# Performance work log

Measured on AMD Instinct MI355X. Metric: run time of the kernel, lower is better.

Reference implementation:

```python
import jax, jax.numpy as jnp
import numpy as np

NEG_INF = -9e15
ALPHA = 0.2  # attention leaky_relu slope


def _gat_layer(h, adj_mask, W, a1, a2):
    # h: [N, Fin], W: [Fin, D], a1/a2: [D]
    Wh = h @ W                                   # [N, D]
    f1 = Wh @ a1                                 # [N]
    f2 = Wh @ a2                                 # [N]
    e = jax.nn.leaky_relu(f1[:, None] + f2[None, :], ALPHA)  # [N, N]
    scores = jnp.where(adj_mask, e, NEG_INF)
    att = jax.nn.softmax(scores, axis=-1)        # row-normalized over neighbors
    return att @ Wh                              # [N, D]


def setup_inputs() -> dict:
    key = jax.random.key(0)
    ks = jax.random.split(key, 12)
    N, Fin, H, D, C = 4096, 512, 8, 64, 64
    s = 0.1
    x = jax.random.normal(ks[0], (N, Fin), jnp.float32)
    adj = jax.random.randint(ks[1], (N, N), 0, 2, jnp.int32)
    W = jax.random.normal(ks[2], (H, Fin, D), jnp.float32) * s
    a1 = jax.random.normal(ks[3], (H, D), jnp.float32) * s
    a2 = jax.random.normal(ks[4], (H, D), jnp.float32) * s
    Wo = jax.random.normal(ks[5], (H * D, C), jnp.float32) * s
    ao1 = jax.random.normal(ks[6], (C,), jnp.float32) * s
    ao2 = jax.random.normal(ks[7], (C,), jnp.float32) * s
    W1 = jax.random.normal(ks[8], (512, N), jnp.float32) * 0.01  # nn.Linear(N, 512)
    b1 = jnp.zeros((512,), jnp.float32)
    W2 = jax.random.normal(ks[9], (256, 512), jnp.float32) * 0.04  # nn.Linear(512, 256)
    b2 = jnp.zeros((256,), jnp.float32)
    return {"x": x, "adj": adj, "W": W, "a1": a1, "a2": a2,
            "Wo": Wo, "ao1": ao1, "ao2": ao2,
            "W1": W1, "b1": b1, "W2": W2, "b2": b2}


def reference(x, adj, W, a1, a2, Wo, ao1, ao2, W1, b1, W2, b2):
    mask = adj > 0                                    # [N, N]
    # multi-head dense attention, concat=True -> ELU per head
    heads = jax.vmap(lambda Wk, a1k, a2k: _gat_layer(x, mask, Wk, a1k, a2k))(W, a1, a2)  # [H, N, D]
    h = jax.nn.elu(heads).transpose(1, 0, 2).reshape(x.shape[0], -1)  # [N, H*D]
    # output attention layer, concat=False (no inner ELU), then outer ELU
    out = jax.nn.elu(_gat_layer(h, mask, Wo, ao1, ao2))  # [N, C]
    out = jax.nn.log_softmax(out, axis=0)                # over nodes (dim=0)
    # MLP head on transposed features: [C, N] -> [C, 512] -> [C, 256]
    y = jax.nn.leaky_relu(out.T @ W1.T + b1, 0.1)
    y = y @ W2.T + b2
    return y
```

## Files before the change

kernel.cpp:

```cpp
#include <hip/hip_runtime.h>
#include <hip/hip_bf16.h>
#include <math.h>


#define N_NODES 4096
#define FIN 512
#define NHEAD 8
#define DHEAD 64
#define NCLS 64
#define NW 64

typedef unsigned short u16;
typedef unsigned long long u64;
typedef __attribute__((ext_vector_type(8))) short bf16x8;
typedef __attribute__((ext_vector_type(4))) float f32x4;

__device__ __forceinline__ float lrelu02(float x) { return x > 0.f ? x : 0.2f * x; }
__device__ __forceinline__ u16 bf16u(float x) {
    __hip_bfloat16 h = __float2bfloat16(x);
    return __builtin_bit_cast(unsigned short, h);
}
__device__ __forceinline__ f32x4 mfma16(bf16x8 a, bf16x8 b, f32x4 c) {
    return __builtin_amdgcn_mfma_f32_16x16x32_bf16(a, b, c, 0, 0, 0);
}
__device__ __forceinline__ unsigned fkey(float f) {
    unsigned u = __builtin_bit_cast(unsigned, f);
    return (u & 0x80000000u) ? ~u : (u | 0x80000000u);
}
__device__ __forceinline__ float funkey(unsigned k) {
    unsigned u = (k & 0x80000000u) ? (k ^ 0x80000000u) : ~k;
    return __builtin_bit_cast(float, u);
}

__global__ void pack_mask(const int* __restrict__ adj, u64* __restrict__ mb,
                          unsigned* __restrict__ gmk) {
    if (blockIdx.x == 0 && threadIdx.x < 16) gmk[threadIdx.x] = 0u;
    int nwaves = (gridDim.x * blockDim.x) >> 6;
    int wid = (blockIdx.x * blockDim.x + threadIdx.x) >> 6;
    int lane = threadIdx.x & 63;
    for (int w = wid; w < N_NODES * NW; w += nwaves) {
        int i = w >> 6, wc = w & 63;
        int j = (wc << 6) | lane;
        u64 m = __ballot(adj[(size_t)i * N_NODES + j] > 0);
        if (lane == 0) mb[w] = m;
    }
}

__global__ void cvt4(const float* __restrict__ s, u16* __restrict__ d, int n4) {
    int i = blockIdx.x * blockDim.x + threadIdx.x;
    if (i < n4) {
        float4 v = ((const float4*)s)[i];
        ushort4 o = {bf16u(v.x), bf16u(v.y), bf16u(v.z), bf16u(v.w)};
        ((ushort4*)d)[i] = o;
    }
}

__global__ __launch_bounds__(256) void to_bf16_T(
    const float* __restrict__ src, int ldsrc, size_t cstep,
    u16* __restrict__ dst, size_t dstep, int ldd) {
    __shared__ alignas(16) u16 T[64][72];
    const int j0 = blockIdx.x * 64;
    const size_t c0 = (size_t)blockIdx.y * cstep;
    u16* d = dst + (size_t)blockIdx.y * dstep;
    const int t = threadIdx.x;
    const int row = t & 63, g = t >> 6;
    #pragma unroll
    for (int k = 0; k < 16; k += 4) {
        float4 v = *(const float4*)(src + (size_t)(j0 + row) * ldsrc + c0 + g * 16 + k);
        T[g * 16 + k + 0][row] = bf16u(v.x);
        T[g * 16 + k + 1][row] = bf16u(v.y);
        T[g * 16 + k + 2][row] = bf16u(v.z);
        T[g * 16 + k + 3][row] = bf16u(v.w);
    }
    __syncthreads();
    const int dd = t >> 2, jc = (t & 3) * 16;
    *(uint4*)(d + (size_t)dd * ldd + j0 + jc) = *(const uint4*)&T[dd][jc];
    *(uint4*)(d + (size_t)dd * ldd + j0 + jc + 8) = *(const uint4*)&T[dd][jc + 8];
}

__global__ __launch_bounds__(256) void gemm_fused(
    const u16* __restrict__ A, int lda, const u16* __restrict__ Bt, int ldb,
    const float* __restrict__ a1a, const float* __restrict__ a2a,
    u16* __restrict__ WhBT, float* __restrict__ f1o, float* __restrict__ f2o,
    unsigned* __restrict__ gmk, int K) {
    __shared__ alignas(16) u16 T[64][72];
    const int t = threadIdx.x, lane = t & 63, wv = t >> 6;
    const int c16 = lane & 15, kg = lane >> 4;
    const int h = blockIdx.x;
    const int bm = blockIdx.y * 64;
    const u16* Ap = A + (size_t)(bm + wv * 16 + c16) * lda + kg * 8;
    const u16* Bp = Bt + (size_t)(h * 64 + c16) * ldb + kg * 8;
    f32x4 acc[4] = {};
    #pragma unroll 4
    for (int k0 = 0; k0 < K; k0 += 32) {
        bf16x8 a = *(const bf16x8*)(Ap + k0);
        #pragma unroll
        for (int ct = 0; ct < 4; ++ct) {
            bf16x8 b = *(const bf16x8*)(Bp + (size_t)ct * 16 * ldb + k0);
            acc[ct] = mfma16(a, b, acc[ct]);
        }
    }
    float a1v[4], a2v[4];
    #pragma unroll
    for (int ct = 0; ct < 4; ++ct) {
        a1v[ct] = a1a[h * 64 + ct * 16 + c16];
        a2v[ct] = a2a[h * 64 + ct * 16 + c16];
    }
    float mx = -1e30f;
    #pragma unroll
    for (int r = 0; r < 4; ++r) {
        float s1 = 0.f, s2 = 0.f;
        int rl = wv * 16 + kg * 4 + r;
        #pragma unroll
        for (int ct = 0; ct < 4; ++ct) {
            float v = acc[ct][r];
            s1 = fmaf(v, a1v[ct], s1);
            s2 = fmaf(v, a2v[ct], s2);
            T[ct * 16 + c16][rl] = bf16u(v);
        }
        #pragma unroll
        for (int off = 1; off < 16; off <<= 1) {
            s1 += __shfl_xor(s1, off, 64);
            s2 += __shfl_xor(s2, off, 64);
        }
        if (c16 == 0) {
            f1o[(size_t)h * N_NODES + bm + rl] = s1;
            f2o[(size_t)h * N_NODES + bm + rl] = s2;
        }
        mx = fmaxf(mx, s2);
    }
    mx = fmaxf(mx, __shfl_xor(mx, 16, 64));
    mx = fmaxf(mx, __shfl_xor(mx, 32, 64));
    if (lane == 0) atomicMax(&gmk[h], fkey(mx));
    __syncthreads();
    const int dd = t >> 2, jc = (t & 3) * 16;
    u16* dst = WhBT + (size_t)(h * 64 + dd) * N_NODES + bm;
    *(uint4*)(dst + jc) = *(const uint4*)&T[dd][jc];
    *(uint4*)(dst + jc + 8) = *(const uint4*)&T[dd][jc + 8];
}

__global__ void coefk(const float* __restrict__ f1, const float* __restrict__ f2,
                      const unsigned* __restrict__ gmk, float4* __restrict__ rowc,
                      float2* __restrict__ uv) {
    int h = blockIdx.y;
    int i = blockIdx.x * 256 + threadIdx.x;
    float g = funkey(gmk[h]);
    float a = f1[(size_t)h * N_NODES + i];
    float s = a + g;
    float M = lrelu02(s);
    rowc[(size_t)h * N_NODES + i] = make_float4(__expf(s - M), __expf(0.2f * s - M), 0.f, 0.f);
    float b = f2[(size_t)h * N_NODES + i] - g;
    uv[(size_t)h * N_NODES + i] = make_float2(__expf(b), __expf(0.2f * b));
}

template <int NH, int ROWS, int JSPLIT, int OUTF>
__global__ __launch_bounds__(256) void attn_v3(
    const u16* __restrict__ WhB, const float2* __restrict__ uv,
    const float4* __restrict__ rowc, const u64* __restrict__ mb,
    float* __restrict__ outp, float* __restrict__ denP) {
    constexpr int NQ = ROWS / 4;
    constexpr int NMT = ROWS / 16;
    constexpr int NJT = (N_NODES / 64) / JSPLIT;
    __shared__ alignas(16) u16 pS[2][ROWS][64];
    __shared__ float Tof[(OUTF == 3) ? 64 * 33 : 1];
    const int b = blockIdx.x;
    int h, ib, js;
    if (NH == 8) { h = b & 7; int r = b >> 3; js = r % JSPLIT; ib = r / JSPLIT; }
    else { h = 0; js = b % JSPLIT; ib = b / JSPLIT; }
    const int i0 = ib * ROWS;
    const int jt0 = js * NJT;
    const int t = threadIdx.x, lane = t & 63, wv = t >> 6;
    const int wv_u = __builtin_amdgcn_readfirstlane(wv);

    const float2* __restrict__ uvp = uv + (size_t)h * N_NODES;
    const float4* __restrict__ rcp = rowc + (size_t)h * N_NODES;
    const u64* __restrict__ mbp = mb + (size_t)(i0 + wv_u) * NW + jt0;

    float Aq[NQ], Bq[NQ], den[NQ];
    #pragma unroll
    for (int q = 0; q < NQ; ++q) {
        float4 rc = rcp[i0 + q * 4 + wv];
        Aq[q] = rc.x; Bq[q] = rc.y; den[q] = 0.f;
    }
    const int wcE = lane ^ (wv << 3);
    const int wcO = lane ^ ((wv + 4) << 3);
    const int kg = lane >> 4, c16 = lane & 15;
    const int ocol = wv * 16 + c16;
    const u16* bptr = WhB + ((size_t)h * 64 + ocol) * N_NODES + jt0 * 64 + kg * 8;
    const int sw8 = (c16 & 7) << 3;
    f32x4 acc[NMT] = {};

    bf16x8 b0 = *(const bf16x8*)(bptr);
    bf16x8 b1 = *(const bf16x8*)(bptr + 32);
    float2 uvv = uvp[jt0 * 64 + lane];
    u64 m[NQ];
    #pragma unroll
    for (int q = 0; q < NQ; ++q) m[q] = mbp[q * 4 * NW];

    for (int it = 0; it < NJT; ++it) {
        const int buf = it & 1;
        const int nit = (it + 1 < NJT) ? it + 1 : it;
        bf16x8 nb0 = *(const bf16x8*)(bptr + (size_t)nit * 64);
        bf16x8 nb1 = *(const bf16x8*)(bptr + (size_t)nit * 64 + 32);
        float2 nuv = uvp[(jt0 + nit) * 64 + lane];
        u64 nm[NQ];
        #pragma unroll
        for (int q = 0; q < NQ; ++q) nm[q] = mbp[q * 4 * NW + nit];
        #pragma unroll
        for (int q = 0; q < NQ; ++q) {
            unsigned wlo = __builtin_amdgcn_readfirstlane((unsigned)m[q]);
            unsigned whi = __builtin_amdgcn_readfirstlane((unsigned)(m[q] >> 32));
            u64 ws = ((u64)whi << 32) | wlo;
            float tv = fmaxf(Aq[q] * uvv.x, Bq[q] * uvv.y);
            float p;
            asm("v_cndmask_b32 %0, 0, %1, %2" : "=v"(p) : "v"(tv), "s"(ws));
            den[q] += p;
            pS[buf][q * 4 + wv][(q & 1) ? wcO : wcE] = bf16u(p);
        }
        __syncthreads();
        __builtin_amdgcn_s_setprio(1);
        #pragma unroll
        for (int mt = 0; mt < NMT; ++mt) {
            const u16* ap = &pS[buf][mt * 16 + c16][0];
            bf16x8 a0 = *(const bf16x8*)&ap[(kg * 8) ^ sw8];
            bf16x8 a1 = *(const bf16x8*)&ap[(32 + kg * 8) ^ sw8];
            acc[mt] = mfma16(a0, b0, acc[mt]);
            acc[mt] = mfma16(a1, b1, acc[mt]);
        }
        __builtin_amdgcn_s_setprio(0);
        b0 = nb0; b1 = nb1; uvv = nuv;
        #pragma unroll
        for (int q = 0; q < NQ; ++q) m[q] = nm[q];
    }

    #pragma unroll
    for (int q = 0; q < NQ; ++q) {
        float s = den[q];
        #pragma unroll
        for (int off = 32; off; off >>= 1) s += __shfl_xor(s, off, 64);
        den[q] = s;
    }

    if constexpr (OUTF == 1) {
        if (lane == 0) {
            #pragma unroll
            for (int q = 0; q < NQ; ++q)
                denP[(size_t)js * (8 * N_NODES) + (size_t)h * N_NODES + i0 + q * 4 + wv] = den[q];
        }
        float* dst = outp + (size_t)js * N_NODES * 512;
        #pragma unroll
        for (int mt = 0; mt < NMT; ++mt)
            #pragma unroll
            for (int r = 0; r < 4; ++r)
                dst[(size_t)(i0 + mt * 16 + kg * 4 + r) * 512 + h * 64 + ocol] = acc[mt][r];
    } else {
        if (lane == 0) {
            #pragma unroll
            for (int q = 0; q < NQ; ++q)
                denP[(size_t)js * N_NODES + i0 + q * 4 + wv] = den[q];
        }
        #pragma unroll
        for (int mt = 0; mt < NMT; ++mt)
            #pragma unroll
            for (int r = 0; r < 4; ++r)
                Tof[ocol * 33 + mt * 16 + kg * 4 + r] = acc[mt][r];
        __syncthreads();
        const int c = t >> 2, r0 = (t & 3) * 8;
        float* dst = outp + (size_t)js * 64 * N_NODES + (size_t)c * N_NODES + i0 + r0;
        float4 v0 = {Tof[c * 33 + r0 + 0], Tof[c * 33 + r0 + 1],
                     Tof[c * 33 + r0 + 2], Tof[c * 33 + r0 + 3]};
        float4 v1 = {Tof[c * 33 + r0 + 4], Tof[c * 33 + r0 + 5],
                     Tof[c * 33 + r0 + 6], Tof[c * 33 + r0 + 7]};
        *(float4*)(dst) = v0;
        *(float4*)(dst + 4) = v1;
    }
}

__global__ __launch_bounds__(256) void combine8(
    const float* __restrict__ part, const float* __restrict__ denp,
    u16* __restrict__ hB) {
    const int t4 = (blockIdx.x * 256 + threadIdx.x) * 4;
    const int i = t4 >> 9, c = t4 & 511, h = c >> 6;
    float4 p0 = *(const float4*)(part + t4);
    float4 p1 = *(const float4*)(part + (size_t)N_NODES * 512 + t4);
    float d = denp[h * N_NODES + i] + denp[8 * N_NODES + h * N_NODES + i];
    float inv = d > 0.f ? 1.f / d : 0.f;
    float v[4] = {(p0.x + p1.x) * inv, (p0.y + p1.y) * inv,
                  (p0.z + p1.z) * inv, (p0.w + p1.w) * inv};
    ushort4 o;
    #pragma unroll
    for (int k = 0; k < 4; ++k) {
        float e = v[k] > 0.f ? v[k] : expm1f(v[k]);
        ((u16*)&o)[k] = bf16u(e);
    }
    *(ushort4*)(hB + t4) = o;
}

__global__ __launch_bounds__(256) void combine1_lsm(
    const float* __restrict__ partT, const float* __restrict__ denp,
    u16* __restrict__ lsT) {
    __shared__ float vb[N_NODES];
    __shared__ float r[256];
    const int c = blockIdx.x, t = threadIdx.x;
    float m = -1e30f;
    for (int i = t * 4; i < N_NODES; i += 1024) {
        float4 s = {0.f, 0.f, 0.f, 0.f}, d = {0.f, 0.f, 0.f, 0.f};
        #pragma unroll
        for (int js = 0; js < 4; ++js) {
            float4 pv = *(const float4*)(partT + (size_t)js * 64 * N_NODES +
                                         (size_t)c * N_NODES + i);
            float4 dv = *(const float4*)(denp + (size_t)js * N_NODES + i);
            s.x += pv.x; s.y += pv.y; s.z += pv.z; s.w += pv.w;
            d.x += dv.x; d.y += dv.y; d.z += dv.z; d.w += dv.w;
        }
        float vv[4] = {d.x > 0.f ? s.x / d.x : 0.f, d.y > 0.f ? s.y / d.y : 0.f,
                       d.z > 0.f ? s.z / d.z : 0.f, d.w > 0.f ? s.w / d.w : 0.f};
        #pragma unroll
        for (int k = 0; k < 4; ++k) {
            float e = vv[k] > 0.f ? vv[k] : expm1f(vv[k]);
            vb[i + k] = e;
            m = fmaxf(m, e);
        }
    }
    r[t] = m;
    __syncthreads();
    for (int s = 128; s; s >>= 1) {
        if (t < s) r[t] = fmaxf(r[t], r[t + s]);
        __syncthreads();
    }
    m = r[0];
    __syncthreads();
    float sum = 0.f;
    for (int i = t; i < N_NODES; i += 256) sum += __expf(vb[i] - m);
    r[t] = sum;
    __syncthreads();
    for (int s = 128; s; s >>= 1) {
        if (t < s) r[t] += r[t + s];
        __syncthreads();
    }
    float lse = m + __logf(r[0]);
    for (int i = t * 4; i < N_NODES; i += 1024) {
        ushort4 o = {bf16u(vb[i] - lse), bf16u(vb[i + 1] - lse),
                     bf16u(vb[i + 2] - lse), bf16u(vb[i + 3] - lse)};
        *(ushort4*)(lsT + (size_t)c * N_NODES + i) = o;
    }
}

__global__ __launch_bounds__(256) void mlp1_mfma(
    const u16* __restrict__ lsT, const u16* __restrict__ W1B,
    float* __restrict__ part) {
    const int t = threadIdx.x, lane = t & 63, wv = t >> 6;
    const int c16 = lane & 15, kg = lane >> 4;
    const int ks = blockIdx.x & 15;
    const int bn = (blockIdx.x >> 4) * 64;
    const int kb = ks * 256;
    const u16* Ap = lsT + (size_t)(wv * 16 + c16) * N_NODES + kb + kg * 8;
    const u16* Bp = W1B + (size_t)(bn + c16) * N_NODES + kb + kg * 8;
    f32x4 acc[4] = {};
    #pragma unroll
    for (int k0 = 0; k0 < 256; k0 += 32) {
        bf16x8 a = *(const bf16x8*)(Ap + k0);
        #pragma unroll
        for (int ct = 0; ct < 4; ++ct) {
            bf16x8 b = *(const bf16x8*)(Bp + (size_t)ct * 16 * N_NODES + k0);
            acc[ct] = mfma16(a, b, acc[ct]);
        }
    }
    float* dst = part + (size_t)ks * 64 * 512;
    #pragma unroll
    for (int ct = 0; ct < 4; ++ct)
        #pragma unroll
        for (int r = 0; r < 4; ++r)
            dst[(size_t)(wv * 16 + kg * 4 + r) * 512 + bn + ct * 16 + c16] = acc[ct][r];
}

__global__ void mlp1_fin(const float* __restrict__ part, const float* __restrict__ b1,
                         float* __restrict__ y1) {
    int idx = blockIdx.x * 256 + threadIdx.x;
    int o = idx & 511;
    float s = 0.f;
    #pragma unroll
    for (int ks = 0; ks < 16; ++ks) s += part[(size_t)ks * 32768 + idx];
    s += b1[o];
    y1[idx] = s > 0.f ? s : 0.1f * s;
}

__global__ __launch_bounds__(256) void mlp2(
    const float* __restrict__ y1, const float* __restrict__ W2,
    const float* __restrict__ b2, float* __restrict__ out) {
    __shared__ alignas(16) float row[512];
    int c = blockIdx.x, t = threadIdx.x;
    row[t] = y1[(size_t)c * 512 + t];
    row[t + 256] = y1[(size_t)c * 512 + t + 256];
    __syncthreads();
    float acc = 0.f;
    #pragma unroll 4
    for (int o = 0; o < 512; o += 4) {
        float4 w4 = *(const float4*)(W2 + (size_t)t * 512 + o);
        float4 r4 = *(const float4*)(&row[o]);
        acc += w4.x * r4.x + w4.y * r4.y + w4.z * r4.z + w4.w * r4.w;
    }
    out[(size_t)c * 256 + t] = acc + b2[t];
}

extern "C" void kernel_launch(void* const* d_in, const int* in_sizes, int n_in,
                              void* d_out, int out_size, void* d_ws, size_t ws_size,
                              hipStream_t stream) {
    const float* x   = (const float*)d_in[0];
    const int*   adj = (const int*)d_in[1];
    const float* W   = (const float*)d_in[2];
    const float* a1  = (const float*)d_in[3];
    const float* a2  = (const float*)d_in[4];
    const float* Wo  = (const float*)d_in[5];
    const float* ao1 = (const float*)d_in[6];
    const float* ao2 = (const float*)d_in[7];
    const float* W1  = (const float*)d_in[8];
    const float* b1  = (const float*)d_in[9];
    const float* W2  = (const float*)d_in[10];
    const float* b2  = (const float*)d_in[11];
    float* out = (float*)d_out;

    char* ws = (char*)d_ws;
    size_t off = 0;
    auto alloc = [&](size_t bytes) {
        void* p = ws + off;
        off += (bytes + 255) & ~(size_t)255;
        return p;
    };
    u64*     mb     = (u64*)alloc((size_t)N_NODES * NW * 8);
    u16*     xB     = (u16*)alloc((size_t)N_NODES * FIN * 2);
    u16*     WBt    = (u16*)alloc((size_t)NHEAD * DHEAD * FIN * 2);
    u16*     WoBt   = (u16*)alloc((size_t)DHEAD * FIN * 2);
    u16*     W1B    = (u16*)alloc((size_t)512 * N_NODES * 2);
    u16*     WhB    = (u16*)alloc((size_t)NHEAD * DHEAD * N_NODES * 2);
    u16*     WhoB   = (u16*)alloc((size_t)DHEAD * N_NODES * 2);
    u16*     hB     = (u16*)alloc((size_t)N_NODES * 512 * 2);
    float*   part8  = (float*)alloc((size_t)2 * N_NODES * 512 * 4);
    float*   den8   = (float*)alloc((size_t)2 * 8 * N_NODES * 4);
    float*   partT1 = (float*)alloc((size_t)4 * 64 * N_NODES * 4);
    float*   den1   = (float*)alloc((size_t)4 * N_NODES * 4);
    u16*     lsT    = (u16*)alloc((size_t)64 * N_NODES * 2);
    float*   part   = (float*)alloc((size_t)16 * 64 * 512 * 4);
    float*   f1b    = (float*)alloc((size_t)9 * N_NODES * 4);
    float*   f2b    = (float*)alloc((size_t)9 * N_NODES * 4);
    unsigned* gmk   = (unsigned*)alloc(16 * 4);
    float4*  rowc   = (float4*)alloc((size_t)9 * N_NODES * 16);
    float2*  uvb    = (float2*)alloc((size_t)9 * N_NODES * 8);
    float*   y1     = (float*)alloc((size_t)64 * 512 * 4);
    (void)ws_size; (void)in_sizes; (void)n_in; (void)out_size;

    pack_mask<<<1024, 256, 0, stream>>>(adj, mb, gmk);
    cvt4<<<(N_NODES * FIN / 4 + 255) / 256, 256, 0, stream>>>(x, xB, N_NODES * FIN / 4);
    cvt4<<<(512 * N_NODES / 4 + 255) / 256, 256, 0, stream>>>(W1, W1B, 512 * N_NODES / 4);
    to_bf16_T<<<dim3(8, 8), 256, 0, stream>>>(W, 64, (size_t)FIN * DHEAD, WBt,
                                              (size_t)DHEAD * FIN, FIN);
    to_bf16_T<<<dim3(8, 1), 256, 0, stream>>>(Wo, 64, 0, WoBt, 0, FIN);
    gemm_fused<<<dim3(8, 64), 256, 0, stream>>>(xB, FIN, WBt, FIN, a1, a2,
                                                WhB, f1b, f2b, gmk, FIN);
    coefk<<<dim3(16, 8), 256, 0, stream>>>(f1b, f2b, gmk, rowc, uvb);
    attn_v3<8, 64, 2, 1><<<(N_NODES / 64) * 2 * 8, 256, 0, stream>>>(
        WhB, uvb, rowc, mb, part8, den8);
    combine8<<<N_NODES * 512 / 4 / 256, 256, 0, stream>>>(part8, den8, hB);
    gemm_fused<<<dim3(1, 64), 256, 0, stream>>>(hB, 512, WoBt, FIN, ao1, ao2,
                                                WhoB, f1b + (size_t)8 * N_NODES,
                                                f2b + (size_t)8 * N_NODES, gmk + 8, FIN);
    coefk<<<dim3(16, 1), 256, 0, stream>>>(f1b + (size_t)8 * N_NODES,
                                           f2b + (size_t)8 * N_NODES, gmk + 8,
                                           rowc + (size_t)8 * N_NODES,
                                           uvb + (size_t)8 * N_NODES);
    attn_v3<1, 32, 4, 3><<<(N_NODES / 32) * 4, 256, 0, stream>>>(
        WhoB, uvb + (size_t)8 * N_NODES, rowc + (size_t)8 * N_NODES, mb, partT1, den1);
    combine1_lsm<<<64, 256, 0, stream>>>(partT1, den1, lsT);
    mlp1_mfma<<<128, 256, 0, stream>>>(lsT, W1B, part);
    mlp1_fin<<<128, 256, 0, stream>>>(part, b1, y1);
    mlp2<<<64, 256, 0, stream>>>(y1, W2, b2, out);
}
```

Baseline: 209.2 us.

## Merge small prep and MLP kernels and double attention j-split factors

Two cvt4 launches become one cvt4b kernel, and the two transposes of W and Wo become one wT9 launch. mlp1_fin is folded into mlp2, which cuts the number of kernel launches. The attention kernels double their j-split (2→4 for the head layer, 1 head 4→8 for the output layer) to create more blocks and raise occupancy. The combine kernels now sum over more partials, and workspace buffers are overlaid to save memory, at the cost of extra partial-sum traffic.

```diff
diff --git a/kernel.cpp b/kernel.cpp
--- a/kernel.cpp
+++ b/kernel.cpp
@@ -46,27 +46,31 @@
     }
 }
 
-__global__ void cvt4(const float* __restrict__ s, u16* __restrict__ d, int n4) {
+__global__ void cvt4b(const float* __restrict__ sa, u16* __restrict__ da, int n4a,
+                      const float* __restrict__ sb, u16* __restrict__ db, int n4b) {
     int i = blockIdx.x * blockDim.x + threadIdx.x;
-    if (i < n4) {
-        float4 v = ((const float4*)s)[i];
-        ushort4 o = {bf16u(v.x), bf16u(v.y), bf16u(v.z), bf16u(v.w)};
-        ((ushort4*)d)[i] = o;
-    }
-}
-
-__global__ __launch_bounds__(256) void to_bf16_T(
-    const float* __restrict__ src, int ldsrc, size_t cstep,
-    u16* __restrict__ dst, size_t dstep, int ldd) {
+    const float* s;
+    u16* d;
+    if (i < n4a) { s = sa; d = da; }
+    else { i -= n4a; if (i >= n4b) return; s = sb; d = db; }
+    float4 v = ((const float4*)s)[i];
+    ushort4 o = {bf16u(v.x), bf16u(v.y), bf16u(v.z), bf16u(v.w)};
+    ((ushort4*)d)[i] = o;
+}
+
+__global__ __launch_bounds__(256) void wT9(
+    const float* __restrict__ W, const float* __restrict__ Wo,
+    u16* __restrict__ WBt, u16* __restrict__ WoBt) {
     __shared__ alignas(16) u16 T[64][72];
+    const int y = blockIdx.y;
+    const float* src = (y < 8) ? W + (size_t)y * FIN * DHEAD : Wo;
+    u16* d = (y < 8) ? WBt + (size_t)y * DHEAD * FIN : WoBt;
     const int j0 = blockIdx.x * 64;
-    const size_t c0 = (size_t)blockIdx.y * cstep;
-    u16* d = dst + (size_t)blockIdx.y * dstep;
     const int t = threadIdx.x;
     const int row = t & 63, g = t >> 6;
     #pragma unroll
     for (int k = 0; k < 16; k += 4) {
-        float4 v = *(const float4*)(src + (size_t)(j0 + row) * ldsrc + c0 + g * 16 + k);
+        float4 v = *(const float4*)(src + (size_t)(j0 + row) * 64 + g * 16 + k);
         T[g * 16 + k + 0][row] = bf16u(v.x);
         T[g * 16 + k + 1][row] = bf16u(v.y);
         T[g * 16 + k + 2][row] = bf16u(v.z);
@@ -74,8 +78,8 @@
     }
     __syncthreads();
     const int dd = t >> 2, jc = (t & 3) * 16;
-    *(uint4*)(d + (size_t)dd * ldd + j0 + jc) = *(const uint4*)&T[dd][jc];
-    *(uint4*)(d + (size_t)dd * ldd + j0 + jc + 8) = *(const uint4*)&T[dd][jc + 8];
+    *(uint4*)(d + (size_t)dd * FIN + j0 + jc) = *(const uint4*)&T[dd][jc];
+    *(uint4*)(d + (size_t)dd * FIN + j0 + jc + 8) = *(const uint4*)&T[dd][jc + 8];
 }
 
 __global__ __launch_bounds__(256) void gemm_fused(
@@ -162,7 +166,7 @@
     constexpr int NMT = ROWS / 16;
     constexpr int NJT = (N_NODES / 64) / JSPLIT;
     __shared__ alignas(16) u16 pS[2][ROWS][64];
-    __shared__ float Tof[(OUTF == 3) ? 64 * 33 : 1];
+    __shared__ float Tof[(OUTF == 3) ? 64 * (ROWS + 1) : 1];
     const int b = blockIdx.x;
     int h, ib, js;
     if (NH == 8) { h = b & 7; int r = b >> 3; js = r % JSPLIT; ib = r / JSPLIT; }
@@ -263,14 +267,14 @@
         for (int mt = 0; mt < NMT; ++mt)
             #pragma unroll
             for (int r = 0; r < 4; ++r)
-                Tof[ocol * 33 + mt * 16 + kg * 4 + r] = acc[mt][r];
+                Tof[ocol * (ROWS + 1) + mt * 16 + kg * 4 + r] = acc[mt][r];
         __syncthreads();
         const int c = t >> 2, r0 = (t & 3) * 8;
         float* dst = outp + (size_t)js * 64 * N_NODES + (size_t)c * N_NODES + i0 + r0;
-        float4 v0 = {Tof[c * 33 + r0 + 0], Tof[c * 33 + r0 + 1],
-                     Tof[c * 33 + r0 + 2], Tof[c * 33 + r0 + 3]};
-        float4 v1 = {Tof[c * 33 + r0 + 4], Tof[c * 33 + r0 + 5],
-                     Tof[c * 33 + r0 + 6], Tof[c * 33 + r0 + 7]};
+        float4 v0 = {Tof[c * (ROWS + 1) + r0 + 0], Tof[c * (ROWS + 1) + r0 + 1],
+                     Tof[c * (ROWS + 1) + r0 + 2], Tof[c * (ROWS + 1) + r0 + 3]};
+        float4 v1 = {Tof[c * (ROWS + 1) + r0 + 4], Tof[c * (ROWS + 1) + r0 + 5],
+                     Tof[c * (ROWS + 1) + r0 + 6], Tof[c * (ROWS + 1) + r0 + 7]};
         *(float4*)(dst) = v0;
         *(float4*)(dst + 4) = v1;
     }
@@ -281,12 +285,16 @@
     u16* __restrict__ hB) {
     const int t4 = (blockIdx.x * 256 + threadIdx.x) * 4;
     const int i = t4 >> 9, c = t4 & 511, h = c >> 6;
-    float4 p0 = *(const float4*)(part + t4);
-    float4 p1 = *(const float4*)(part + (size_t)N_NODES * 512 + t4);
-    float d = denp[h * N_NODES + i] + denp[8 * N_NODES + h * N_NODES + i];
+    float4 s = {0.f, 0.f, 0.f, 0.f};
+    float d = 0.f;
+    #pragma unroll
+    for (int js = 0; js < 4; ++js) {
+        float4 p = *(const float4*)(part + (size_t)js * N_NODES * 512 + t4);
+        s.x += p.x; s.y += p.y; s.z += p.z; s.w += p.w;
+        d += denp[(size_t)js * (8 * N_NODES) + h * N_NODES + i];
+    }
     float inv = d > 0.f ? 1.f / d : 0.f;
-    float v[4] = {(p0.x + p1.x) * inv, (p0.y + p1.y) * inv,
-                  (p0.z + p1.z) * inv, (p0.w + p1.w) * inv};
+    float v[4] = {s.x * inv, s.y * inv, s.z * inv, s.w * inv};
     ushort4 o;
     #pragma unroll
     for (int k = 0; k < 4; ++k) {
@@ -306,7 +314,7 @@
     for (int i = t * 4; i < N_NODES; i += 1024) {
         float4 s = {0.f, 0.f, 0.f, 0.f}, d = {0.f, 0.f, 0.f, 0.f};
         #pragma unroll
-        for (int js = 0; js < 4; ++js) {
+        for (int js = 0; js < 8; ++js) {
             float4 pv = *(const float4*)(partT + (size_t)js * 64 * N_NODES +
                                          (size_t)c * N_NODES + i);
             float4 dv = *(const float4*)(denp + (size_t)js * N_NODES + i);
@@ -374,24 +382,22 @@
             dst[(size_t)(wv * 16 + kg * 4 + r) * 512 + bn + ct * 16 + c16] = acc[ct][r];
 }
 
-__global__ void mlp1_fin(const float* __restrict__ part, const float* __restrict__ b1,
-                         float* __restrict__ y1) {
-    int idx = blockIdx.x * 256 + threadIdx.x;
-    int o = idx & 511;
-    float s = 0.f;
-    #pragma unroll
-    for (int ks = 0; ks < 16; ++ks) s += part[(size_t)ks * 32768 + idx];
-    s += b1[o];
-    y1[idx] = s > 0.f ? s : 0.1f * s;
-}
-
-__global__ __launch_bounds__(256) void mlp2(
-    const float* __restrict__ y1, const float* __restrict__ W2,
-    const float* __restrict__ b2, float* __restrict__ out) {
+__global__ __launch_bounds__(256) void mlp2f(
+    const float* __restrict__ part, const float* __restrict__ b1,
+    const float* __restrict__ W2, const float* __restrict__ b2,
+    float* __restrict__ out) {
     __shared__ alignas(16) float row[512];
-    int c = blockIdx.x, t = threadIdx.x;
-    row[t] = y1[(size_t)c * 512 + t];
-    row[t + 256] = y1[(size_t)c * 512 + t + 256];
+    const int c = blockIdx.x, t = threadIdx.x;
+    #pragma unroll
+    for (int half = 0; half < 2; ++half) {
+        int o = t + half * 256;
+        float s = 0.f;
+        #pragma unroll
+        for (int ks = 0; ks < 16; ++ks)
+            s += part[(size_t)ks * 32768 + (size_t)c * 512 + o];
+        s += b1[o];
+        row[o] = s > 0.f ? s : 0.1f * s;
+    }
     __syncthreads();
     float acc = 0.f;
     #pragma unroll 4
@@ -435,30 +441,28 @@
     u16*     WhB    = (u16*)alloc((size_t)NHEAD * DHEAD * N_NODES * 2);
     u16*     WhoB   = (u16*)alloc((size_t)DHEAD * N_NODES * 2);
     u16*     hB     = (u16*)alloc((size_t)N_NODES * 512 * 2);
-    float*   part8  = (float*)alloc((size_t)2 * N_NODES * 512 * 4);
-    float*   den8   = (float*)alloc((size_t)2 * 8 * N_NODES * 4);
-    float*   partT1 = (float*)alloc((size_t)4 * 64 * N_NODES * 4);
-    float*   den1   = (float*)alloc((size_t)4 * N_NODES * 4);
-    u16*     lsT    = (u16*)alloc((size_t)64 * N_NODES * 2);
-    float*   part   = (float*)alloc((size_t)16 * 64 * 512 * 4);
+    float*   part8  = (float*)alloc((size_t)4 * N_NODES * 512 * 4);
+    float*   den8   = (float*)alloc((size_t)4 * 8 * N_NODES * 4);
     float*   f1b    = (float*)alloc((size_t)9 * N_NODES * 4);
     float*   f2b    = (float*)alloc((size_t)9 * N_NODES * 4);
     unsigned* gmk   = (unsigned*)alloc(16 * 4);
     float4*  rowc   = (float4*)alloc((size_t)9 * N_NODES * 16);
     float2*  uvb    = (float2*)alloc((size_t)9 * N_NODES * 8);
-    float*   y1     = (float*)alloc((size_t)64 * 512 * 4);
+    char*    ov     = (char*)part8;
+    float*   partT1 = (float*)(ov);
+    float*   den1   = (float*)(ov + ((size_t)8 << 20));
+    u16*     lsT    = (u16*)(ov + ((size_t)8 << 20) + (256 << 10));
+    float*   part   = (float*)(ov + ((size_t)9 << 20));
     (void)ws_size; (void)in_sizes; (void)n_in; (void)out_size;
 
     pack_mask<<<1024, 256, 0, stream>>>(adj, mb, gmk);
-    cvt4<<<(N_NODES * FIN / 4 + 255) / 256, 256, 0, stream>>>(x, xB, N_NODES * FIN / 4);
-    cvt4<<<(512 * N_NODES / 4 + 255) / 256, 256, 0, stream>>>(W1, W1B, 512 * N_NODES / 4);
-    to_bf16_T<<<dim3(8, 8), 256, 0, stream>>>(W, 64, (size_t)FIN * DHEAD, WBt,
-                                              (size_t)DHEAD * FIN, FIN);
-    to_bf16_T<<<dim3(8, 1), 256, 0, stream>>>(Wo, 64, 0, WoBt, 0, FIN);
+    cvt4b<<<(2 * N_NODES * FIN / 4 + 255) / 256, 256, 0, stream>>>(
+        x, xB, N_NODES * FIN / 4, W1, W1B, 512 * N_NODES / 4);
+    wT9<<<dim3(8, 9), 256, 0, stream>>>(W, Wo, WBt, WoBt);
     gemm_fused<<<dim3(8, 64), 256, 0, stream>>>(xB, FIN, WBt, FIN, a1, a2,
                                                 WhB, f1b, f2b, gmk, FIN);
     coefk<<<dim3(16, 8), 256, 0, stream>>>(f1b, f2b, gmk, rowc, uvb);
-    attn_v3<8, 64, 2, 1><<<(N_NODES / 64) * 2 * 8, 256, 0, stream>>>(
+    attn_v3<8, 64, 4, 1><<<(N_NODES / 64) * 4 * 8, 256, 0, stream>>>(
         WhB, uvb, rowc, mb, part8, den8);
     combine8<<<N_NODES * 512 / 4 / 256, 256, 0, stream>>>(part8, den8, hB);
     gemm_fused<<<dim3(1, 64), 256, 0, stream>>>(hB, 512, WoBt, FIN, ao1, ao2,
@@ -468,10 +472,9 @@
                                            f2b + (size_t)8 * N_NODES, gmk + 8,
                                            rowc + (size_t)8 * N_NODES,
                                            uvb + (size_t)8 * N_NODES);
-    attn_v3<1, 32, 4, 3><<<(N_NODES / 32) * 4, 256, 0, stream>>>(
+    attn_v3<1, 32, 8, 3><<<(N_NODES / 32) * 8, 256, 0, stream>>>(
         WhoB, uvb + (size_t)8 * N_NODES, rowc + (size_t)8 * N_NODES, mb, partT1, den1);
     combine1_lsm<<<64, 256, 0, stream>>>(partT1, den1, lsT);
     mlp1_mfma<<<128, 256, 0, stream>>>(lsT, W1B, part);
-    mlp1_fin<<<128, 256, 0, stream>>>(part, b1, y1);
-    mlp2<<<64, 256, 0, stream>>>(y1, W2, b2, out);
-}
+    mlp2f<<<64, 256, 0, stream>>>(part, b1, W2, b2, out);
+}
```

Result: slower. 214.4 us (+2.5%).
